# Optimization experiments

Hardware: AMD Instinct MI355X
Metric: run time of the kernel (lower is better)

Reference implementation:

```python
import jax, jax.numpy as jnp
import numpy as np

NEG_INF = -1e9


def setup_inputs() -> dict:
    key0 = jax.random.key(0)
    ks = jax.random.split(key0, 7)
    B, Tq, Tv, D, U = 8, 512, 512, 512, 128
    query = jax.random.normal(ks[0], (B, Tq, D), dtype=jnp.float32)
    key = jax.random.normal(ks[1], (B, Tv, D), dtype=jnp.float32)
    value = jax.random.normal(ks[2], (B, Tv, D), dtype=jnp.float32)
    mask = jax.random.randint(ks[3], (B, Tv), 0, 2).astype(bool)
    mask = mask.at[:, 0].set(True)  # ensure no fully-masked row
    Wa = jax.random.normal(ks[4], (D, U), dtype=jnp.float32) * (1.0 / np.sqrt(D))
    Ua = jax.random.normal(ks[5], (D, U), dtype=jnp.float32) * (1.0 / np.sqrt(D))
    scale = jax.random.normal(ks[6], (U,), dtype=jnp.float32) * 0.1
    return {"query": query, "key": key, "value": value, "mask": mask,
            "Wa": Wa, "Ua": Ua, "scale": scale}


def reference(query, key, value, mask, Wa, Ua, scale):
    # Dense projections (no bias)
    q = query @ Wa          # [B, Tq, U]
    k = key @ Ua            # [B, Tv, U]
    # Additive (Bahdanau) scores with learned per-unit scale:
    # scores[b,i,j] = sum_u scale[u] * tanh(q[b,i,u] + k[b,j,u])
    t = jnp.tanh(q[:, :, None, :] + k[:, None, :, :])   # [B, Tq, Tv, U]
    scores = jnp.einsum('bijU,U->bij', t, scale)         # [B, Tq, Tv]
    # Mask padded keys/values then softmax over Tv
    scores = jnp.where(mask[:, None, :], scores, NEG_INF)
    weights = jax.nn.softmax(scores, axis=-1)            # [B, Tq, Tv]
    # Weighted sum of values (query_mask is all-True in source -> no-op)
    context = jnp.einsum('bij,bjd->bid', weights, value) # [B, Tq, D]
    return context
```

## Files before the change

kernel.cpp:

```cpp
#include <hip/hip_runtime.h>

constexpr int Bb = 8;
constexpr int Tq = 512;
constexpr int Tv = 512;
constexpr int Dd = 512;
constexpr int Uu = 128;
constexpr float C2LOG2E = 2.88539008177792681f;

typedef float v2f __attribute__((ext_vector_type(2)));

__global__ __launch_bounds__(512, 8) void proj_kernel(
    const float* __restrict__ query,
    const float* __restrict__ key,
    const float* __restrict__ Wa,
    const float* __restrict__ Ua,
    const int* __restrict__ mask,
    float* __restrict__ qf2, float* __restrict__ kT,
    int* __restrict__ jl_g, int* __restrict__ cnt_g)
{
    const int R    = blockIdx.x * 8;
    const bool isQ = R < Bb * Tq;
    const float* __restrict__ src = isQ ? query : key;
    const float* __restrict__ W   = isQ ? Wa : Ua;
    const int Rloc = isQ ? R : R - Bb * Tq;

    __shared__ float part[8 * 8 * 128];
    __shared__ int posLoc[8];
    const int t = threadIdx.x;

    if (!isQ && t < 64) {
        const int b  = Rloc >> 9;
        const int j0 = Rloc & 511;
        const bool writer = (j0 == 0);
        int base = 0;
#pragma unroll
        for (int c = 0; c < 8; ++c) {
            const int j = c * 64 + t;
            const int v = (mask[b * 512 + j] != 0);
            const unsigned long long bits = __ballot(v);
            const int pos = base + (int)__popcll(bits & ((1ull << t) - 1ull));
            if (j >= j0 && j < j0 + 8) posLoc[j - j0] = v ? pos : -1;
            if (writer && v) jl_g[b * 512 + pos] = j;
            base += (int)__popcll(bits);
        }
        if (writer && t == 0) cnt_g[b] = base;
    }

    const int u2 = (t & 63) * 2;
    const int dq = __builtin_amdgcn_readfirstlane(t >> 6);
    const float* __restrict__ Wq = W + (size_t)dq * 64 * Uu;
    const float* __restrict__ xs = src + (size_t)Rloc * Dd + dq * 64;

    float acc[8][2];
#pragma unroll
    for (int r = 0; r < 8; ++r) { acc[r][0] = 0.f; acc[r][1] = 0.f; }

#pragma unroll 2
    for (int d4 = 0; d4 < 16; ++d4) {
        const int d = d4 * 4;
        const float2 w0 = *reinterpret_cast<const float2*>(Wq + (d + 0) * Uu + u2);
        const float2 w1 = *reinterpret_cast<const float2*>(Wq + (d + 1) * Uu + u2);
        const float2 w2 = *reinterpret_cast<const float2*>(Wq + (d + 2) * Uu + u2);
        const float2 w3 = *reinterpret_cast<const float2*>(Wq + (d + 3) * Uu + u2);
#pragma unroll
        for (int r = 0; r < 8; ++r) {
            const float4 xv = *reinterpret_cast<const float4*>(xs + r * Dd + d);
            acc[r][0] = fmaf(xv.x, w0.x, acc[r][0]);
            acc[r][1] = fmaf(xv.x, w0.y, acc[r][1]);
            acc[r][0] = fmaf(xv.y, w1.x, acc[r][0]);
            acc[r][1] = fmaf(xv.y, w1.y, acc[r][1]);
            acc[r][0] = fmaf(xv.z, w2.x, acc[r][0]);
            acc[r][1] = fmaf(xv.z, w2.y, acc[r][1]);
            acc[r][0] = fmaf(xv.w, w3.x, acc[r][0]);
            acc[r][1] = fmaf(xv.w, w3.y, acc[r][1]);
        }
    }

    {
#pragma unroll
        for (int r = 0; r < 8; ++r) {
            float2 p; p.x = acc[r][0]; p.y = acc[r][1];
            *reinterpret_cast<float2*>(part + (dq * 8 + r) * 128 + u2) = p;
        }
    }
    __syncthreads();

    {
        const int r  = t >> 6;
        const int u0 = (t & 63) * 2;
        float s0 = 0.f, s1 = 0.f;
#pragma unroll
        for (int p = 0; p < 8; ++p) {
            const float2 pv = *reinterpret_cast<const float2*>(part + (p * 8 + r) * 128 + u0);
            s0 += pv.x;
            s1 += pv.y;
        }
        float2 e;
        e.x = __builtin_amdgcn_exp2f(C2LOG2E * s0);
        e.y = __builtin_amdgcn_exp2f(C2LOG2E * s1);
        if (isQ) {
            *reinterpret_cast<float2*>(qf2 + (size_t)(Rloc + r) * Uu + u0) = e;
        } else {
            const int p = posLoc[r];
            if (p >= 0) {
                float* __restrict__ kb = kT + (size_t)(Rloc >> 9) * Uu * Tv;
                const int u4 = u0 >> 2;
                const int c  = u0 & 3;
                *reinterpret_cast<float2*>(kb + ((size_t)u4 * Tv + p) * 4 + c) = e;
            }
        }
    }
}

__global__ __launch_bounds__(512, 8) void attn_kernel(
    const float* __restrict__ qf2, const float* __restrict__ kT,
    const float* __restrict__ value,
    const int* __restrict__ jl_g, const int* __restrict__ cnt_g,
    const float* __restrict__ scale,
    float* __restrict__ out)
{
    const int bid = blockIdx.x;
    const int swz = (bid & 7) * 128 + (bid >> 3);
    const int r0 = swz * 4;
    const int b  = r0 >> 9;
    const int t  = threadIdx.x;

    __shared__ int   jl[Tv];
    __shared__ float w[4 * Tv];
    __shared__ float pbuf[12 * Dd];
    __shared__ float sums8[8];

    const int cnt = cnt_g[b];
    jl[t] = (t < cnt) ? jl_g[b * 512 + t] : 0;

    const int wvu = __builtin_amdgcn_readfirstlane(t >> 6);
    const int cntp4 = (cnt + 3) & ~3;

    {
        const int g   = wvu >> 2;
        const int jc0 = t & 255;
        const float* __restrict__ qs = qf2 + (size_t)r0 * Uu + g * 64;
        const float* __restrict__ ss = scale + g * 64;
        const float4* __restrict__ kb4 =
            reinterpret_cast<const float4*>(kT) + (size_t)b * 32 * Tv + (size_t)g * 16 * Tv;
        float* __restrict__ wr = g ? pbuf : w;
        for (int jb = 0; jb < cnt; jb += 256) {
            const int jc = jb + jc0;
            if (jc < cnt) {
                v2f acc2[4];
#pragma unroll
                for (int i = 0; i < 4; ++i) acc2[i] = (v2f){0.f, 0.f};
#pragma unroll 4
                for (int u4 = 0; u4 < 16; ++u4) {
                    const float4 kv = kb4[(size_t)u4 * Tv + jc];
                    const v2f kv01 = {kv.x, kv.y};
                    const v2f kv23 = {kv.z, kv.w};
                    const v2f sv01 = *reinterpret_cast<const v2f*>(ss + u4 * 4);
                    const v2f sv23 = *reinterpret_cast<const v2f*>(ss + u4 * 4 + 2);
#pragma unroll
                    for (int i = 0; i < 4; ++i) {
                        const v2f qv01 = *reinterpret_cast<const v2f*>(qs + i * Uu + u4 * 4);
                        const v2f qv23 = *reinterpret_cast<const v2f*>(qs + i * Uu + u4 * 4 + 2);
                        const v2f one2 = {1.f, 1.f};
                        const v2f p01 = __builtin_elementwise_fma(kv01, qv01, one2);
                        const v2f p23 = __builtin_elementwise_fma(kv23, qv23, one2);
                        const float pp0 = p01.x * p01.y;
                        const float pp1 = p23.x * p23.y;
                        const float r   = __builtin_amdgcn_rcpf(pp0 * pp1);
                        const float r01 = r * pp1;
                        const float r23 = r * pp0;
                        const v2f inv01 = {r01 * p01.y, r01 * p01.x};
                        const v2f inv23 = {r23 * p23.y, r23 * p23.x};
                        acc2[i] = __builtin_elementwise_fma(sv01, inv01, acc2[i]);
                        acc2[i] = __builtin_elementwise_fma(sv23, inv23, acc2[i]);
                    }
                }
#pragma unroll
                for (int i = 0; i < 4; ++i) wr[i * Tv + jc] = acc2[i].x + acc2[i].y;
            }
        }
    }
    __syncthreads();

    {
        const int ln = t & 63;
        const int i = wvu >> 1, h = wvu & 1;
        float* __restrict__ row        = w    + i * Tv;
        const float* __restrict__ rowB = pbuf + i * Tv;
        float sum = 0.f;
#pragma unroll
        for (int c = 0; c < 4; ++c) {
            const int e = ln + 64 * (h * 4 + c);
            if (e < cnt) {
                const float ex = __builtin_amdgcn_exp2f(-C2LOG2E * (row[e] + rowB[e]));
                row[e] = ex;
                sum += ex;
            } else {
                row[e] = 0.f;
            }
        }
#pragma unroll
        for (int off = 32; off; off >>= 1) sum += __shfl_xor(sum, off, 64);
        if (ln == 0) sums8[wvu] = sum;
    }
    __syncthreads();

    const int g2 = wvu >> 1;
    const int cc = t & 127;
    const int d0 = cc * 4;
    const int chunk = ((cntp4 + 15) >> 4) << 2;
    const int jbeg = g2 * chunk;
    const int jend = min(jbeg + chunk, cntp4);
    const float* __restrict__ vb = value + (size_t)b * Tv * Dd + d0;
    v2f axl[4], axh[4];
#pragma unroll
    for (int i = 0; i < 4; ++i) { axl[i] = (v2f){0.f, 0.f}; axh[i] = (v2f){0.f, 0.f}; }

#pragma unroll 2
    for (int jj = jbeg; jj < jend; jj += 4) {
        const int4 rows = *reinterpret_cast<const int4*>(jl + jj);
        const float4 v0 = *reinterpret_cast<const float4*>(vb + (size_t)rows.x * Dd);
        const float4 v1 = *reinterpret_cast<const float4*>(vb + (size_t)rows.y * Dd);
        const float4 v2 = *reinterpret_cast<const float4*>(vb + (size_t)rows.z * Dd);
        const float4 v3 = *reinterpret_cast<const float4*>(vb + (size_t)rows.w * Dd);
        const v2f v0l = {v0.x, v0.y}, v0h = {v0.z, v0.w};
        const v2f v1l = {v1.x, v1.y}, v1h = {v1.z, v1.w};
        const v2f v2l = {v2.x, v2.y}, v2h = {v2.z, v2.w};
        const v2f v3l = {v3.x, v3.y}, v3h = {v3.z, v3.w};
#pragma unroll
        for (int i = 0; i < 4; ++i) {
            const float4 wq = *reinterpret_cast<const float4*>(w + i * Tv + jj);
            const v2f wx = {wq.x, wq.x};
            axl[i] = __builtin_elementwise_fma(wx, v0l, axl[i]);
            axh[i] = __builtin_elementwise_fma(wx, v0h, axh[i]);
            const v2f wy = {wq.y, wq.y};
            axl[i] = __builtin_elementwise_fma(wy, v1l, axl[i]);
            axh[i] = __builtin_elementwise_fma(wy, v1h, axh[i]);
            const v2f wz = {wq.z, wq.z};
            axl[i] = __builtin_elementwise_fma(wz, v2l, axl[i]);
            axh[i] = __builtin_elementwise_fma(wz, v2h, axh[i]);
            const v2f ww = {wq.w, wq.w};
            axl[i] = __builtin_elementwise_fma(ww, v3l, axl[i]);
            axh[i] = __builtin_elementwise_fma(ww, v3h, axh[i]);
        }
    }

    if (g2 != 0) {
#pragma unroll
        for (int i = 0; i < 4; ++i) {
            const float4 p = make_float4(axl[i].x, axl[i].y, axh[i].x, axh[i].y);
            *reinterpret_cast<float4*>(pbuf + ((size_t)(g2 - 1) * 4 + i) * Dd + d0) = p;
        }
    }
    __syncthreads();
    if (g2 == 0) {
#pragma unroll
        for (int i = 0; i < 4; ++i) {
            const float inv = 1.0f / (sums8[2 * i] + sums8[2 * i + 1]);
            const float4 p1 = *reinterpret_cast<const float4*>(pbuf + ((size_t)0 * 4 + i) * Dd + d0);
            const float4 p2 = *reinterpret_cast<const float4*>(pbuf + ((size_t)1 * 4 + i) * Dd + d0);
            const float4 p3 = *reinterpret_cast<const float4*>(pbuf + ((size_t)2 * 4 + i) * Dd + d0);
            float4 o;
            o.x = (axl[i].x + p1.x + p2.x + p3.x) * inv;
            o.y = (axl[i].y + p1.y + p2.y + p3.y) * inv;
            o.z = (axh[i].x + p1.z + p2.z + p3.z) * inv;
            o.w = (axh[i].y + p1.w + p2.w + p3.w) * inv;
            *reinterpret_cast<float4*>(out + (size_t)(r0 + i) * Dd + d0) = o;
        }
    }
}

extern "C" void kernel_launch(void* const* d_in, const int* in_sizes, int n_in,
                              void* d_out, int out_size, void* d_ws, size_t ws_size,
                              hipStream_t stream)
{
    const float* query = (const float*)d_in[0];
    const float* key   = (const float*)d_in[1];
    const float* value = (const float*)d_in[2];
    const int*   mask  = (const int*)d_in[3];
    const float* Wa    = (const float*)d_in[4];
    const float* Ua    = (const float*)d_in[5];
    const float* scale = (const float*)d_in[6];
    float* out = (float*)d_out;

    float* qf2 = (float*)d_ws;
    float* kT  = qf2 + Bb * Tq * Uu;
    int*   jl_g  = (int*)(kT + Bb * Uu * Tv);
    int*   cnt_g = jl_g + Bb * Tv;

    proj_kernel<<<(2 * Bb * Tq) / 8, 512, 0, stream>>>(query, key, Wa, Ua, mask,
                                                       qf2, kT, jl_g, cnt_g);
    attn_kernel<<<(Bb * Tq) / 4, 512, 0, stream>>>(qf2, kT, value, jl_g, cnt_g,
                                                   scale, out);
}
```

Measured before the change: 143.1 us.

## Fuse query projection into attention kernel, shrink key projection blocks

Moves the query projection (query @ Wa followed by exp) out of the projection kernel and into the attention kernel, where each block computes its 4 query rows into shared memory. This removes the qf2 workspace round trip and halves the work of the first kernel, which now projects only keys with 4 rows per block instead of 8. The cost is extra per-block startup latency and two extra syncs in the attention kernel before scoring begins. It also adds a small shared-memory buffer, which could affect occupancy.

```diff
diff --git a/kernel.cpp b/kernel.cpp
--- a/kernel.cpp
+++ b/kernel.cpp
@@ -9,27 +9,21 @@
 
 typedef float v2f __attribute__((ext_vector_type(2)));
 
-__global__ __launch_bounds__(512, 8) void proj_kernel(
-    const float* __restrict__ query,
+__global__ __launch_bounds__(512, 8) void kproj_kernel(
     const float* __restrict__ key,
-    const float* __restrict__ Wa,
     const float* __restrict__ Ua,
     const int* __restrict__ mask,
-    float* __restrict__ qf2, float* __restrict__ kT,
+    float* __restrict__ kT,
     int* __restrict__ jl_g, int* __restrict__ cnt_g)
 {
-    const int R    = blockIdx.x * 8;
-    const bool isQ = R < Bb * Tq;
-    const float* __restrict__ src = isQ ? query : key;
-    const float* __restrict__ W   = isQ ? Wa : Ua;
-    const int Rloc = isQ ? R : R - Bb * Tq;
-
-    __shared__ float part[8 * 8 * 128];
-    __shared__ int posLoc[8];
+    const int Rloc = blockIdx.x * 4;
+    const int b    = Rloc >> 9;
+
+    __shared__ float part[8 * 4 * 128];
+    __shared__ int posLoc[4];
     const int t = threadIdx.x;
 
-    if (!isQ && t < 64) {
-        const int b  = Rloc >> 9;
+    if (t < 64) {
         const int j0 = Rloc & 511;
         const bool writer = (j0 == 0);
         int base = 0;
@@ -39,7 +33,7 @@
             const int v = (mask[b * 512 + j] != 0);
             const unsigned long long bits = __ballot(v);
             const int pos = base + (int)__popcll(bits & ((1ull << t) - 1ull));
-            if (j >= j0 && j < j0 + 8) posLoc[j - j0] = v ? pos : -1;
+            if (j >= j0 && j < j0 + 4) posLoc[j - j0] = v ? pos : -1;
             if (writer && v) jl_g[b * 512 + pos] = j;
             base += (int)__popcll(bits);
         }
@@ -48,12 +42,12 @@
 
     const int u2 = (t & 63) * 2;
     const int dq = __builtin_amdgcn_readfirstlane(t >> 6);
-    const float* __restrict__ Wq = W + (size_t)dq * 64 * Uu;
-    const float* __restrict__ xs = src + (size_t)Rloc * Dd + dq * 64;
-
-    float acc[8][2];
-#pragma unroll
-    for (int r = 0; r < 8; ++r) { acc[r][0] = 0.f; acc[r][1] = 0.f; }
+    const float* __restrict__ Wq = Ua + (size_t)dq * 64 * Uu;
+    const float* __restrict__ xs = key + (size_t)Rloc * Dd + dq * 64;
+
+    float acc[4][2];
+#pragma unroll
+    for (int r = 0; r < 4; ++r) { acc[r][0] = 0.f; acc[r][1] = 0.f; }
 
 #pragma unroll 2
     for (int d4 = 0; d4 < 16; ++d4) {
@@ -63,7 +57,7 @@
         const float2 w2 = *reinterpret_cast<const float2*>(Wq + (d + 2) * Uu + u2);
         const float2 w3 = *reinterpret_cast<const float2*>(Wq + (d + 3) * Uu + u2);
 #pragma unroll
-        for (int r = 0; r < 8; ++r) {
+        for (int r = 0; r < 4; ++r) {
             const float4 xv = *reinterpret_cast<const float4*>(xs + r * Dd + d);
             acc[r][0] = fmaf(xv.x, w0.x, acc[r][0]);
             acc[r][1] = fmaf(xv.x, w0.y, acc[r][1]);
@@ -76,45 +70,31 @@
         }
     }
 
-    {
-#pragma unroll
-        for (int r = 0; r < 8; ++r) {
-            float2 p; p.x = acc[r][0]; p.y = acc[r][1];
-            *reinterpret_cast<float2*>(part + (dq * 8 + r) * 128 + u2) = p;
-        }
-    }
-    __syncthreads();
-
-    {
-        const int r  = t >> 6;
-        const int u0 = (t & 63) * 2;
-        float s0 = 0.f, s1 = 0.f;
-#pragma unroll
-        for (int p = 0; p < 8; ++p) {
-            const float2 pv = *reinterpret_cast<const float2*>(part + (p * 8 + r) * 128 + u0);
-            s0 += pv.x;
-            s1 += pv.y;
-        }
-        float2 e;
-        e.x = __builtin_amdgcn_exp2f(C2LOG2E * s0);
-        e.y = __builtin_amdgcn_exp2f(C2LOG2E * s1);
-        if (isQ) {
-            *reinterpret_cast<float2*>(qf2 + (size_t)(Rloc + r) * Uu + u0) = e;
-        } else {
-            const int p = posLoc[r];
-            if (p >= 0) {
-                float* __restrict__ kb = kT + (size_t)(Rloc >> 9) * Uu * Tv;
-                const int u4 = u0 >> 2;
-                const int c  = u0 & 3;
-                *reinterpret_cast<float2*>(kb + ((size_t)u4 * Tv + p) * 4 + c) = e;
-            }
+#pragma unroll
+    for (int r = 0; r < 4; ++r) {
+        float2 p; p.x = acc[r][0]; p.y = acc[r][1];
+        *reinterpret_cast<float2*>(part + (dq * 4 + r) * 128 + u2) = p;
+    }
+    __syncthreads();
+
+    {
+        const int r = t >> 7;
+        const int u = t & 127;
+        float s = 0.f;
+#pragma unroll
+        for (int p = 0; p < 8; ++p) s += part[(p * 4 + r) * 128 + u];
+        const float e = __builtin_amdgcn_exp2f(C2LOG2E * s);
+        const int pos = posLoc[r];
+        if (pos >= 0) {
+            float* __restrict__ kb = kT + (size_t)b * Uu * Tv;
+            kb[((size_t)(u >> 2) * Tv + pos) * 4 + (u & 3)] = e;
         }
     }
 }
 
 __global__ __launch_bounds__(512, 8) void attn_kernel(
-    const float* __restrict__ qf2, const float* __restrict__ kT,
-    const float* __restrict__ value,
+    const float* __restrict__ query, const float* __restrict__ Wa,
+    const float* __restrict__ kT, const float* __restrict__ value,
     const int* __restrict__ jl_g, const int* __restrict__ cnt_g,
     const float* __restrict__ scale,
     float* __restrict__ out)
@@ -128,6 +108,7 @@
     __shared__ int   jl[Tv];
     __shared__ float w[4 * Tv];
     __shared__ float pbuf[12 * Dd];
+    __shared__ float qe[4 * Uu];
     __shared__ float sums8[8];
 
     const int cnt = cnt_g[b];
@@ -137,9 +118,53 @@
     const int cntp4 = (cnt + 3) & ~3;
 
     {
+        const int u2 = (t & 63) * 2;
+        const float* __restrict__ Wq = Wa + (size_t)wvu * 64 * Uu;
+        const float* __restrict__ xs = query + (size_t)r0 * Dd + wvu * 64;
+        float acc[4][2];
+#pragma unroll
+        for (int r = 0; r < 4; ++r) { acc[r][0] = 0.f; acc[r][1] = 0.f; }
+#pragma unroll 2
+        for (int d4 = 0; d4 < 16; ++d4) {
+            const int d = d4 * 4;
+            const float2 w0 = *reinterpret_cast<const float2*>(Wq + (d + 0) * Uu + u2);
+            const float2 w1 = *reinterpret_cast<const float2*>(Wq + (d + 1) * Uu + u2);
+            const float2 w2 = *reinterpret_cast<const float2*>(Wq + (d + 2) * Uu + u2);
+            const float2 w3 = *reinterpret_cast<const float2*>(Wq + (d + 3) * Uu + u2);
+#pragma unroll
+            for (int r = 0; r < 4; ++r) {
+                const float4 xv = *reinterpret_cast<const float4*>(xs + r * Dd + d);
+                acc[r][0] = fmaf(xv.x, w0.x, acc[r][0]);
+                acc[r][1] = fmaf(xv.x, w0.y, acc[r][1]);
+                acc[r][0] = fmaf(xv.y, w1.x, acc[r][0]);
+                acc[r][1] = fmaf(xv.y, w1.y, acc[r][1]);
+                acc[r][0] = fmaf(xv.z, w2.x, acc[r][0]);
+                acc[r][1] = fmaf(xv.z, w2.y, acc[r][1]);
+                acc[r][0] = fmaf(xv.w, w3.x, acc[r][0]);
+                acc[r][1] = fmaf(xv.w, w3.y, acc[r][1]);
+            }
+        }
+#pragma unroll
+        for (int r = 0; r < 4; ++r) {
+            float2 p; p.x = acc[r][0]; p.y = acc[r][1];
+            *reinterpret_cast<float2*>(pbuf + (wvu * 4 + r) * 128 + u2) = p;
+        }
+    }
+    __syncthreads();
+    {
+        const int r = t >> 7;
+        const int u = t & 127;
+        float s = 0.f;
+#pragma unroll
+        for (int p = 0; p < 8; ++p) s += pbuf[(p * 4 + r) * 128 + u];
+        qe[r * Uu + u] = __builtin_amdgcn_exp2f(C2LOG2E * s);
+    }
+    __syncthreads();
+
+    {
         const int g   = wvu >> 2;
         const int jc0 = t & 255;
-        const float* __restrict__ qs = qf2 + (size_t)r0 * Uu + g * 64;
+        const float* __restrict__ qs = qe + g * 64;
         const float* __restrict__ ss = scale + g * 64;
         const float4* __restrict__ kb4 =
             reinterpret_cast<const float4*>(kT) + (size_t)b * 32 * Tv + (size_t)g * 16 * Tv;
@@ -283,13 +308,11 @@
     const float* scale = (const float*)d_in[6];
     float* out = (float*)d_out;
 
-    float* qf2 = (float*)d_ws;
-    float* kT  = qf2 + Bb * Tq * Uu;
+    float* kT    = (float*)d_ws;
     int*   jl_g  = (int*)(kT + Bb * Uu * Tv);
     int*   cnt_g = jl_g + Bb * Tv;
 
-    proj_kernel<<<(2 * Bb * Tq) / 8, 512, 0, stream>>>(query, key, Wa, Ua, mask,
-                                                       qf2, kT, jl_g, cnt_g);
-    attn_kernel<<<(Bb * Tq) / 4, 512, 0, stream>>>(qf2, kT, value, jl_g, cnt_g,
-                                                   scale, out);
+    kproj_kernel<<<(Bb * Tv) / 4, 512, 0, stream>>>(key, Ua, mask, kT, jl_g, cnt_g);
+    attn_kernel<<<(Bb * Tq) / 4, 512, 0, stream>>>(query, Wa, kT, value,
+                                                   jl_g, cnt_g, scale, out);
 }
```

Result: slower. 152.1 us (+6.3%).

## Compact masked value rows in projection and widen attention blocks to eight queries

Applied to the files above, without the earlier changes.

The projection kernel now copies unmasked value rows into a compacted per-batch buffer and zero-pads the tail, so the attention kernel reads contiguous value rows instead of gathering through an index list. The attention kernel moves to 1024-thread blocks handling 8 query rows each, with the score computation split four ways over the unit dimension. This doubles reuse of key and value loads per block. The cost is an extra value copy pass in the first kernel, about 64KB of shared memory per block, and higher register pressure with 8 accumulators.

```diff
diff --git a/kernel.cpp b/kernel.cpp
--- a/kernel.cpp
+++ b/kernel.cpp
@@ -12,11 +12,12 @@
 __global__ __launch_bounds__(512, 8) void proj_kernel(
     const float* __restrict__ query,
     const float* __restrict__ key,
+    const float* __restrict__ value,
     const float* __restrict__ Wa,
     const float* __restrict__ Ua,
     const int* __restrict__ mask,
     float* __restrict__ qf2, float* __restrict__ kT,
-    int* __restrict__ jl_g, int* __restrict__ cnt_g)
+    float* __restrict__ vc, int* __restrict__ cnt_g)
 {
     const int R    = blockIdx.x * 8;
     const bool isQ = R < Bb * Tq;
@@ -26,6 +27,7 @@
 
     __shared__ float part[8 * 8 * 128];
     __shared__ int posLoc[8];
+    __shared__ int cntS;
     const int t = threadIdx.x;
 
     if (!isQ && t < 64) {
@@ -40,10 +42,9 @@
             const unsigned long long bits = __ballot(v);
             const int pos = base + (int)__popcll(bits & ((1ull << t) - 1ull));
             if (j >= j0 && j < j0 + 8) posLoc[j - j0] = v ? pos : -1;
-            if (writer && v) jl_g[b * 512 + pos] = j;
             base += (int)__popcll(bits);
         }
-        if (writer && t == 0) cnt_g[b] = base;
+        if (writer && t == 0) { cnt_g[b] = base; cntS = base; }
     }
 
     const int u2 = (t & 63) * 2;
@@ -110,55 +111,78 @@
             }
         }
     }
+
+    if (!isQ) {
+        const int b = Rloc >> 9;
+        {
+            const int r  = t >> 6;
+            const int di = t & 63;
+            const int p  = posLoc[r];
+            if (p >= 0) {
+                const float4* __restrict__ vsrc =
+                    reinterpret_cast<const float4*>(value + (size_t)(Rloc + r) * Dd);
+                float4* __restrict__ vdst =
+                    reinterpret_cast<float4*>(vc + ((size_t)b * Tv + p) * Dd);
+                vdst[di]      = vsrc[di];
+                vdst[di + 64] = vsrc[di + 64];
+            }
+        }
+        if ((Rloc & 511) == 0) {
+            const int cnt = cntS;
+            const int zr = t >> 7;
+            const int zd = t & 127;
+            if (cnt + zr < 512) {
+                float4* __restrict__ vdst =
+                    reinterpret_cast<float4*>(vc + ((size_t)b * Tv + cnt + zr) * Dd);
+                vdst[zd] = make_float4(0.f, 0.f, 0.f, 0.f);
+            }
+        }
+    }
 }
 
-__global__ __launch_bounds__(512, 8) void attn_kernel(
+__global__ __launch_bounds__(1024, 8) void attn_kernel(
     const float* __restrict__ qf2, const float* __restrict__ kT,
-    const float* __restrict__ value,
-    const int* __restrict__ jl_g, const int* __restrict__ cnt_g,
+    const float* __restrict__ vc,
+    const int* __restrict__ cnt_g,
     const float* __restrict__ scale,
     float* __restrict__ out)
 {
     const int bid = blockIdx.x;
-    const int swz = (bid & 7) * 128 + (bid >> 3);
-    const int r0 = swz * 4;
+    const int swz = (bid & 7) * 64 + (bid >> 3);
+    const int r0 = swz * 8;
     const int b  = r0 >> 9;
     const int t  = threadIdx.x;
 
-    __shared__ int   jl[Tv];
-    __shared__ float w[4 * Tv];
-    __shared__ float pbuf[12 * Dd];
-    __shared__ float sums8[8];
+    __shared__ float wbuf[4][8 * Tv];
+    __shared__ float sums16[16];
 
     const int cnt = cnt_g[b];
-    jl[t] = (t < cnt) ? jl_g[b * 512 + t] : 0;
-
     const int wvu = __builtin_amdgcn_readfirstlane(t >> 6);
     const int cntp4 = (cnt + 3) & ~3;
 
     {
         const int g   = wvu >> 2;
         const int jc0 = t & 255;
-        const float* __restrict__ qs = qf2 + (size_t)r0 * Uu + g * 64;
-        const float* __restrict__ ss = scale + g * 64;
+        const float* __restrict__ qs = qf2 + (size_t)r0 * Uu + g * 32;
+        const float* __restrict__ ss = scale + g * 32;
         const float4* __restrict__ kb4 =
-            reinterpret_cast<const float4*>(kT) + (size_t)b * 32 * Tv + (size_t)g * 16 * Tv;
-        float* __restrict__ wr = g ? pbuf : w;
+            reinterpret_cast<const float4*>(kT) + (size_t)b * 32 * Tv + (size_t)g * 8 * Tv;
+        float* __restrict__ wr = wbuf[g];
         for (int jb = 0; jb < cnt; jb += 256) {
             const int jc = jb + jc0;
             if (jc < cnt) {
-                v2f acc2[4];
-#pragma unroll
-                for (int i = 0; i < 4; ++i) acc2[i] = (v2f){0.f, 0.f};
-#pragma unroll 4
-                for (int u4 = 0; u4 < 16; ++u4) {
+                v2f acc2[8];
+#pragma unroll
+                for (int i = 0; i < 8; ++i) acc2[i] = (v2f){0.f, 0.f};
+#pragma unroll 2
+                for (int u4 = 0; u4 < 8; ++u4) {
                     const float4 kv = kb4[(size_t)u4 * Tv + jc];
                     const v2f kv01 = {kv.x, kv.y};
                     const v2f kv23 = {kv.z, kv.w};
                     const v2f sv01 = *reinterpret_cast<const v2f*>(ss + u4 * 4);
                     const v2f sv23 = *reinterpret_cast<const v2f*>(ss + u4 * 4 + 2);
 #pragma unroll
-                    for (int i = 0; i < 4; ++i) {
+                    for (int i = 0; i < 8; ++i) {
                         const v2f qv01 = *reinterpret_cast<const v2f*>(qs + i * Uu + u4 * 4);
                         const v2f qv23 = *reinterpret_cast<const v2f*>(qs + i * Uu + u4 * 4 + 2);
                         const v2f one2 = {1.f, 1.f};
@@ -176,7 +200,7 @@
                     }
                 }
 #pragma unroll
-                for (int i = 0; i < 4; ++i) wr[i * Tv + jc] = acc2[i].x + acc2[i].y;
+                for (int i = 0; i < 8; ++i) wr[i * Tv + jc] = acc2[i].x + acc2[i].y;
             }
         }
     }
@@ -185,14 +209,17 @@
     {
         const int ln = t & 63;
         const int i = wvu >> 1, h = wvu & 1;
-        float* __restrict__ row        = w    + i * Tv;
-        const float* __restrict__ rowB = pbuf + i * Tv;
+        float* __restrict__ row        = wbuf[0] + i * Tv;
+        const float* __restrict__ rowB = wbuf[1] + i * Tv;
+        const float* __restrict__ rowC = wbuf[2] + i * Tv;
+        const float* __restrict__ rowD = wbuf[3] + i * Tv;
         float sum = 0.f;
 #pragma unroll
         for (int c = 0; c < 4; ++c) {
             const int e = ln + 64 * (h * 4 + c);
             if (e < cnt) {
-                const float ex = __builtin_amdgcn_exp2f(-C2LOG2E * (row[e] + rowB[e]));
+                const float ex = __builtin_amdgcn_exp2f(
+                    -C2LOG2E * (row[e] + rowB[e] + rowC[e] + rowD[e]));
                 row[e] = ex;
                 sum += ex;
             } else {
@@ -201,71 +228,54 @@
         }
 #pragma unroll
         for (int off = 32; off; off >>= 1) sum += __shfl_xor(sum, off, 64);
-        if (ln == 0) sums8[wvu] = sum;
+        if (ln == 0) sums16[wvu] = sum;
     }
     __syncthreads();
 
-    const int g2 = wvu >> 1;
-    const int cc = t & 127;
-    const int d0 = cc * 4;
+    const int g2 = wvu >> 2;
+    const int c  = t & 255;
+    const int d0 = c * 2;
     const int chunk = ((cntp4 + 15) >> 4) << 2;
     const int jbeg = g2 * chunk;
     const int jend = min(jbeg + chunk, cntp4);
-    const float* __restrict__ vb = value + (size_t)b * Tv * Dd + d0;
-    v2f axl[4], axh[4];
-#pragma unroll
-    for (int i = 0; i < 4; ++i) { axl[i] = (v2f){0.f, 0.f}; axh[i] = (v2f){0.f, 0.f}; }
+    const float* __restrict__ vb = vc + (size_t)b * Tv * Dd + d0;
+    v2f ax[8];
+#pragma unroll
+    for (int i = 0; i < 8; ++i) ax[i] = (v2f){0.f, 0.f};
 
 #pragma unroll 2
     for (int jj = jbeg; jj < jend; jj += 4) {
-        const int4 rows = *reinterpret_cast<const int4*>(jl + jj);
-        const float4 v0 = *reinterpret_cast<const float4*>(vb + (size_t)rows.x * Dd);
-        const float4 v1 = *reinterpret_cast<const float4*>(vb + (size_t)rows.y * Dd);
-        const float4 v2 = *reinterpret_cast<const float4*>(vb + (size_t)rows.z * Dd);
-        const float4 v3 = *reinterpret_cast<const float4*>(vb + (size_t)rows.w * Dd);
-        const v2f v0l = {v0.x, v0.y}, v0h = {v0.z, v0.w};
-        const v2f v1l = {v1.x, v1.y}, v1h = {v1.z, v1.w};
-        const v2f v2l = {v2.x, v2.y}, v2h = {v2.z, v2.w};
-        const v2f v3l = {v3.x, v3.y}, v3h = {v3.z, v3.w};
-#pragma unroll
-        for (int i = 0; i < 4; ++i) {
-            const float4 wq = *reinterpret_cast<const float4*>(w + i * Tv + jj);
-            const v2f wx = {wq.x, wq.x};
-            axl[i] = __builtin_elementwise_fma(wx, v0l, axl[i]);
-            axh[i] = __builtin_elementwise_fma(wx, v0h, axh[i]);
-            const v2f wy = {wq.y, wq.y};
-            axl[i] = __builtin_elementwise_fma(wy, v1l, axl[i]);
-            axh[i] = __builtin_elementwise_fma(wy, v1h, axh[i]);
-            const v2f wz = {wq.z, wq.z};
-            axl[i] = __builtin_elementwise_fma(wz, v2l, axl[i]);
-            axh[i] = __builtin_elementwise_fma(wz, v2h, axh[i]);
-            const v2f ww = {wq.w, wq.w};
-            axl[i] = __builtin_elementwise_fma(ww, v3l, axl[i]);
-            axh[i] = __builtin_elementwise_fma(ww, v3h, axh[i]);
+        const v2f v0 = *reinterpret_cast<const v2f*>(vb + (size_t)(jj + 0) * Dd);
+        const v2f v1 = *reinterpret_cast<const v2f*>(vb + (size_t)(jj + 1) * Dd);
+        const v2f v2 = *reinterpret_cast<const v2f*>(vb + (size_t)(jj + 2) * Dd);
+        const v2f v3 = *reinterpret_cast<const v2f*>(vb + (size_t)(jj + 3) * Dd);
+#pragma unroll
+        for (int i = 0; i < 8; ++i) {
+            const float4 wq = *reinterpret_cast<const float4*>(wbuf[0] + i * Tv + jj);
+            ax[i] = __builtin_elementwise_fma((v2f){wq.x, wq.x}, v0, ax[i]);
+            ax[i] = __builtin_elementwise_fma((v2f){wq.y, wq.y}, v1, ax[i]);
+            ax[i] = __builtin_elementwise_fma((v2f){wq.z, wq.z}, v2, ax[i]);
+            ax[i] = __builtin_elementwise_fma((v2f){wq.w, wq.w}, v3, ax[i]);
         }
     }
 
     if (g2 != 0) {
 #pragma unroll
-        for (int i = 0; i < 4; ++i) {
-            const float4 p = make_float4(axl[i].x, axl[i].y, axh[i].x, axh[i].y);
-            *reinterpret_cast<float4*>(pbuf + ((size_t)(g2 - 1) * 4 + i) * Dd + d0) = p;
-        }
+        for (int i = 0; i < 8; ++i)
+            *reinterpret_cast<v2f*>(wbuf[g2] + i * Tv + d0) = ax[i];
     }
     __syncthreads();
     if (g2 == 0) {
 #pragma unroll
-        for (int i = 0; i < 4; ++i) {
-            const float inv = 1.0f / (sums8[2 * i] + sums8[2 * i + 1]);
-            const float4 p1 = *reinterpret_cast<const float4*>(pbuf + ((size_t)0 * 4 + i) * Dd + d0);
-            const float4 p2 = *reinterpret_cast<const float4*>(pbuf + ((size_t)1 * 4 + i) * Dd + d0);
-            const float4 p3 = *reinterpret_cast<const float4*>(pbuf + ((size_t)2 * 4 + i) * Dd + d0);
-            float4 o;
-            o.x = (axl[i].x + p1.x + p2.x + p3.x) * inv;
-            o.y = (axl[i].y + p1.y + p2.y + p3.y) * inv;
-            o.z = (axh[i].x + p1.z + p2.z + p3.z) * inv;
-            o.w = (axh[i].y + p1.w + p2.w + p3.w) * inv;
-            *reinterpret_cast<float4*>(out + (size_t)(r0 + i) * Dd + d0) = o;
+        for (int i = 0; i < 8; ++i) {
+            const float inv = 1.0f / (sums16[2 * i] + sums16[2 * i + 1]);
+            const v2f p1 = *reinterpret_cast<const v2f*>(wbuf[1] + i * Tv + d0);
+            const v2f p2 = *reinterpret_cast<const v2f*>(wbuf[2] + i * Tv + d0);
+            const v2f p3 = *reinterpret_cast<const v2f*>(wbuf[3] + i * Tv + d0);
+            float2 o;
+            o.x = (ax[i].x + p1.x + p2.x + p3.x) * inv;
+            o.y = (ax[i].y + p1.y + p2.y + p3.y) * inv;
+            *reinterpret_cast<float2*>(out + (size_t)(r0 + i) * Dd + d0) = o;
         }
     }
 }
@@ -283,13 +293,12 @@
     const float* scale = (const float*)d_in[6];
     float* out = (float*)d_out;
 
-    float* qf2 = (float*)d_ws;
-    float* kT  = qf2 + Bb * Tq * Uu;
-    int*   jl_g  = (int*)(kT + Bb * Uu * Tv);
-    int*   cnt_g = jl_g + Bb * Tv;
-
-    proj_kernel<<<(2 * Bb * Tq) / 8, 512, 0, stream>>>(query, key, Wa, Ua, mask,
-                                                       qf2, kT, jl_g, cnt_g);
-    attn_kernel<<<(Bb * Tq) / 4, 512, 0, stream>>>(qf2, kT, value, jl_g, cnt_g,
-                                                   scale, out);
+    float* qf2   = (float*)d_ws;
+    float* kT    = qf2 + Bb * Tq * Uu;
+    float* vc    = kT + Bb * Uu * Tv;
+    int*   cnt_g = (int*)(vc + (size_t)Bb * Tv * Dd);
+
+    proj_kernel<<<(2 * Bb * Tq) / 8, 512, 0, stream>>>(query, key, value, Wa, Ua,
+                                                       mask, qf2, kT, vc, cnt_g);
+    attn_kernel<<<(Bb * Tq) / 8, 1024, 0, stream>>>(qf2, kT, vc, cnt_g, scale, out);
 }
```

New measurement: 138.2 us. 3.4% less time.
